# Kernel tuning notes

Hardware: AMD Instinct MI355X
Metric: run time of the kernel (lower is better)

The kernel has to match this reference:

```python
import jax, jax.numpy as jnp
import numpy as np

B, N, NH, E = 4, 4096, 16, 64
MD, FF, H, PE = 128, 256, 4, 32
DH = MD // H
SCALE = 1.0 / np.float32(np.sqrt(DH))


def _ln(x, g, b, eps=1e-5):
    m = jnp.mean(x, axis=-1, keepdims=True)
    v = jnp.var(x, axis=-1, keepdims=True)
    return (x - m) * jax.lax.rsqrt(v + eps) * g + b


def setup_inputs() -> dict:
    key = jax.random.key(0)
    ks = jax.random.split(key, 16)
    rn = lambda k, shape: jax.random.normal(k, shape, dtype=jnp.float32) * 0.02
    return {
        "x": jax.random.normal(ks[0], (B, N, NH, E), dtype=jnp.float32),
        "pos1": jax.random.normal(ks[1], (B, N, NH, NH), dtype=jnp.float32),
        "pos2": jax.random.normal(ks[2], (B, N, NH, NH), dtype=jnp.float32),
        # input_mlp: Linear(E->MD, no bias) + LayerNorm
        "W_in": rn(ks[3], (E, MD)), "g_in": jnp.ones((MD,), jnp.float32), "b_in": jnp.zeros((MD,), jnp.float32),
        # pos_embedder (simple MLP on stacked rel-coords) + emb_proj_bias (PE->H, no bias)
        "W_pe": rn(ks[4], (2, PE)),
        "W_bias": rn(ks[5], (PE, H)),
        # MHA qkv projections (with bias) and output projection
        "Wq": rn(ks[6], (MD, MD)), "bq": jnp.zeros((MD,), jnp.float32),
        "Wk": rn(ks[7], (MD, MD)), "bk": jnp.zeros((MD,), jnp.float32),
        "Wv": rn(ks[8], (MD, MD)), "bv": jnp.zeros((MD,), jnp.float32),
        "Wo": rn(ks[9], (MD, MD)), "bo": jnp.zeros((MD,), jnp.float32),
        # mlp_layer: Linear(MD->FF,no bias), SiLU, Linear(FF->MD,no bias)
        "W1": rn(ks[10], (MD, FF)), "W2": rn(ks[11], (FF, MD)),
        "g1": jnp.ones((MD,), jnp.float32), "b1": jnp.zeros((MD,), jnp.float32),
        "g2": jnp.ones((MD,), jnp.float32), "b2": jnp.zeros((MD,), jnp.float32),
    }


def reference(x, pos1, pos2, W_in, g_in, b_in, W_pe, W_bias,
              Wq, bq, Wk, bk, Wv, bv, Wo, bo, W1, W2, g1, b1, g2, b2):
    b, n, nh, _ = x.shape
    # input_mlp
    h = _ln(x @ W_in, g_in, b_in)                      # [b,n,nh,MD]
    t = h.reshape(b * n, nh, MD)                       # windows of nh tokens
    # relative-position bias: pos_embedder then emb_proj_bias
    pe = jax.nn.silu(jnp.stack([pos1, pos2], axis=-1).reshape(b * n, nh, nh, 2) @ W_pe)  # [bn,nh,nh,PE]
    bias = pe @ W_bias                                  # [bn,nh,nh,H]
    # MHA with additive bias
    q = (t @ Wq + bq).reshape(b * n, nh, H, DH)
    k = (t @ Wk + bk).reshape(b * n, nh, H, DH)
    v = (t @ Wv + bv).reshape(b * n, nh, H, DH)
    scores = jnp.einsum('bqhd,bkhd->bhqk', q, k) * SCALE + jnp.transpose(bias, (0, 3, 1, 2))
    att = jax.nn.softmax(scores, axis=-1)               # [bn,H,nh,nh]
    o = jnp.einsum('bhqk,bkhd->bqhd', att, v).reshape(b * n, nh, MD)
    att_out = o @ Wo + bo
    # residual (q_res=True, dropout=0) + norms + FFN
    y = _ln(t + att_out, g1, b1)
    y = _ln(y + jax.nn.silu(y @ W1) @ W2, g2, b2)
    return y.reshape(b, n, nh, MD)
```

## Files before the change

### kernel.cpp

```cpp
#include <hip/hip_runtime.h>
#include <hip/hip_bf16.h>
#include <math.h>

#define NHT 16
#define MD 128
#define FFD 256
#define NHEAD 4
#define DH 32
#define PED 32
#define ED 64
#define SCALE 0.17677669529663687f
#define SCB 136
#define LDT 132
#define SCUF 264

typedef __attribute__((ext_vector_type(8))) short bf8;
typedef __attribute__((ext_vector_type(4))) float f32x4;
union U8 { bf8 v; unsigned short s[8]; uint u[4]; uint4 q; };

#define MFMA __builtin_amdgcn_mfma_f32_16x16x32_bf16

__device__ __forceinline__ unsigned short bf1(float a){
  __hip_bfloat16 h = __float2bfloat16(a);
  return *reinterpret_cast<unsigned short*>(&h);
}
__device__ __forceinline__ float bfh2f(unsigned short s){
  __hip_bfloat16 h = *reinterpret_cast<__hip_bfloat16*>(&s);
  return __bfloat162float(h);
}
__device__ __forceinline__ float silu_f(float x){ return x / (1.f + __expf(-x)); }

__device__ __forceinline__ void lnC(float (&C)[8][4], const float* __restrict__ g,
                                    const float* __restrict__ b, int lm){
#pragma unroll
  for (int r = 0; r < 4; ++r){
    float s = 0.f, ss = 0.f;
#pragma unroll
    for (int nt = 0; nt < 8; ++nt){ s += C[nt][r]; ss = fmaf(C[nt][r], C[nt][r], ss); }
#pragma unroll
    for (int m = 1; m < 16; m <<= 1){ s += __shfl_xor(s, m); ss += __shfl_xor(ss, m); }
    float mean = s * (1.f/128.f);
    float var  = ss * (1.f/128.f) - mean*mean;
    float rs   = rsqrtf(var + 1e-5f);
#pragma unroll
    for (int nt = 0; nt < 8; ++nt)
      C[nt][r] = fmaf((C[nt][r] - mean) * rs, g[nt*16+lm], b[nt*16+lm]);
  }
}

__global__ __launch_bounds__(256)
void packw(const float* __restrict__ Wq, const float* __restrict__ Wk,
           const float* __restrict__ Wv, const float* __restrict__ Wo,
           const float* __restrict__ W1, const float* __restrict__ W2,
           uint4* __restrict__ ws){
  int id = blockIdx.x * 256 + threadIdx.x;
  const float* W; int KT, N, u; uint4* dst;
  if      (id < 2048) { W = Wq;  KT = 4; N = 128; dst = ws;         u = id;         }
  else if (id < 4096) { W = Wk;  KT = 4; N = 128; dst = ws + 2048;  u = id - 2048;  }
  else if (id < 6144) { W = Wv;  KT = 4; N = 128; dst = ws + 4096;  u = id - 4096;  }
  else if (id < 8192) { W = Wo;  KT = 4; N = 128; dst = ws + 6144;  u = id - 6144;  }
  else if (id < 12288){ W = W1;  KT = 4; N = 256; dst = ws + 8192;  u = id - 8192;  }
  else                { W = W2;  KT = 8; N = 128; dst = ws + 12288; u = id - 12288; }
  int lane = u & 63, tile = u >> 6;
  int kt = tile % KT, nt = tile / KT;
  int kr  = kt*32 + ((lane >> 4) << 3);
  int col = nt*16 + (lane & 15);
  const float* p = W + (size_t)kr * N + col;
  U8 hi;
#pragma unroll
  for (int j = 0; j < 8; ++j) hi.s[j] = bf1(p[(size_t)j * N]);
  dst[u] = hi.q;
}

__global__ __launch_bounds__(256)
void packwin(const float* __restrict__ Win, uint4* __restrict__ ws){
  int u = blockIdx.x * 256 + threadIdx.x;
  int lane = u & 63, tile = u >> 6;
  int kt = tile % 2, nt = tile / 2;
  int kr  = kt*32 + ((lane >> 4) << 3);
  int col = nt*16 + (lane & 15);
  const float* p = Win + (size_t)kr * MD + col;
  U8 hi;
#pragma unroll
  for (int j = 0; j < 8; ++j) hi.s[j] = bf1(p[(size_t)j * MD]);
  ws[16384 + u] = hi.q;
}

__global__ __launch_bounds__(64)
void nha_mfma(const float* __restrict__ x, const float* __restrict__ pos1,
              const float* __restrict__ pos2,
              const float* __restrict__ W_in,
              const float* __restrict__ g_in, const float* __restrict__ b_in,
              const float* __restrict__ W_pe, const float* __restrict__ W_bias,
              const float* __restrict__ bq, const float* __restrict__ bk,
              const float* __restrict__ bv, const float* __restrict__ bo,
              const float* __restrict__ g1, const float* __restrict__ b1,
              const float* __restrict__ g2, const float* __restrict__ b2,
              const uint4* __restrict__ wsp, int useWin, float* __restrict__ out)
{
  const uint4* pWq  = wsp;
  const uint4* pWk  = wsp + 2048;
  const uint4* pWv  = wsp + 4096;
  const uint4* pWo  = wsp + 6144;
  const uint4* pW1  = wsp + 8192;
  const uint4* pW2  = wsp + 12288;
  const uint4* pWin = wsp + 16384;

  __shared__ __align__(16) unsigned short Qb[NHT*SCB];
  __shared__ __align__(16) float Kf[NHT*LDT];
  __shared__ __align__(16) float Vf[NHT*LDT];
  __shared__ __align__(16) unsigned short Tb[NHT*SCB];
  __shared__ __align__(16) unsigned short Ub[NHT*SCUF];
  __shared__ __align__(16) float Bsm[NHEAD*NHT*NHT];

  const int tid = threadIdx.x;
  const int wi  = blockIdx.x;
  const int lm  = tid & 15;
  const int lg  = tid >> 4;
  const f32x4 zero4 = {0.f,0.f,0.f,0.f};

  bf8 xA[2];
  {
    const float* xp = x + (size_t)wi*1024 + lm*ED + lg*8;
#pragma unroll
    for (int kt = 0; kt < 2; ++kt){
      U8 h;
#pragma unroll
      for (int j = 0; j < 8; ++j) h.s[j] = bf1(xp[kt*32 + j]);
      xA[kt] = h.v;
    }
  }
  float tC[8][4];
#pragma unroll
  for (int nt = 0; nt < 8; ++nt){
    f32x4 acc = zero4;
#pragma unroll
    for (int kt = 0; kt < 2; ++kt){
      U8 w;
      if (useWin){
        w.q = pWin[(nt*2+kt)*64 + tid];
      } else {
        const float* wp = W_in + (size_t)(kt*32 + lg*8)*MD + nt*16 + lm;
#pragma unroll
        for (int j = 0; j < 8; ++j) w.s[j] = bf1(wp[(size_t)j*MD]);
      }
      acc = MFMA(xA[kt], w.v, acc, 0,0,0);
    }
#pragma unroll
    for (int r = 0; r < 4; ++r) tC[nt][r] = acc[r];
  }
  lnC(tC, g_in, b_in, lm);

#pragma unroll
  for (int nt = 0; nt < 8; ++nt)
#pragma unroll
    for (int r = 0; r < 4; ++r)
      Tb[(lg*4+r)*SCB + nt*16+lm] = bf1(tC[nt][r]);
  __syncthreads();
  bf8 tA[4];
#pragma unroll
  for (int kt = 0; kt < 4; ++kt)
    tA[kt] = *(const bf8*)(Tb + lm*SCB + kt*32 + lg*8);
  __syncthreads();

#pragma unroll
  for (int nt = 0; nt < 8; ++nt){
    float bb = bq[nt*16+lm];
    f32x4 acc = {bb,bb,bb,bb};
#pragma unroll
    for (int kt = 0; kt < 4; ++kt){
      U8 bh; bh.q = pWq[(nt*4+kt)*64 + tid];
      acc = MFMA(tA[kt], bh.v, acc, 0,0,0);
    }
#pragma unroll
    for (int r = 0; r < 4; ++r) Qb[(lg*4+r)*SCB + nt*16+lm] = bf1(acc[r]);
  }
#pragma unroll
  for (int nt = 0; nt < 8; ++nt){
    float bb = bk[nt*16+lm];
    f32x4 acc = {bb,bb,bb,bb};
#pragma unroll
    for (int kt = 0; kt < 4; ++kt){
      U8 bh; bh.q = pWk[(nt*4+kt)*64 + tid];
      acc = MFMA(tA[kt], bh.v, acc, 0,0,0);
    }
#pragma unroll
    for (int r = 0; r < 4; ++r) Kf[(lg*4+r)*LDT + nt*16+lm] = acc[r];
  }
#pragma unroll
  for (int nt = 0; nt < 8; ++nt){
    float bb = bv[nt*16+lm];
    f32x4 acc = {bb,bb,bb,bb};
#pragma unroll
    for (int kt = 0; kt < 4; ++kt){
      U8 bh; bh.q = pWv[(nt*4+kt)*64 + tid];
      acc = MFMA(tA[kt], bh.v, acc, 0,0,0);
    }
#pragma unroll
    for (int r = 0; r < 4; ++r) Vf[(lg*4+r)*LDT + nt*16+lm] = acc[r];
  }

  for (int p = tid; p < NHT*NHT; p += 64){
    float p1 = pos1[(size_t)wi*256 + p];
    float p2 = pos2[(size_t)wi*256 + p];
    float a0=0.f, a1=0.f, a2=0.f, a3=0.f;
#pragma unroll
    for (int i = 0; i < PED; ++i){
      float e = fmaf(p1, W_pe[i], p2 * W_pe[PED+i]);
      float sv = silu_f(e);
      a0 = fmaf(sv, W_bias[i*4+0], a0);
      a1 = fmaf(sv, W_bias[i*4+1], a1);
      a2 = fmaf(sv, W_bias[i*4+2], a2);
      a3 = fmaf(sv, W_bias[i*4+3], a3);
    }
    Bsm[0*256 + p] = a0; Bsm[1*256 + p] = a1; Bsm[2*256 + p] = a2; Bsm[3*256 + p] = a3;
  }
  __syncthreads();

  {
    const int h  = tid >> 4;
    const int qi = tid & 15;
    float qf[DH];
    {
      const unsigned short* qp = Qb + qi*SCB + h*DH;
#pragma unroll
      for (int d0 = 0; d0 < DH; d0 += 8){
        U8 u; u.v = *(const bf8*)(qp + d0);
#pragma unroll
        for (int j = 0; j < 8; ++j) qf[d0+j] = bfh2f(u.s[j]);
      }
    }
    float sc[NHT];
#pragma unroll
    for (int ki = 0; ki < NHT; ++ki){
      const float* krow = Kf + ki*LDT + h*DH;
      float dot = 0.f;
#pragma unroll
      for (int d = 0; d < DH; d += 4){
        float4 kv = *(const float4*)(krow + d);
        dot = fmaf(qf[d], kv.x, dot);   dot = fmaf(qf[d+1], kv.y, dot);
        dot = fmaf(qf[d+2], kv.z, dot); dot = fmaf(qf[d+3], kv.w, dot);
      }
      sc[ki] = fmaf(dot, SCALE, Bsm[h*256 + qi*16 + ki]);
    }
    float mx = sc[0];
#pragma unroll
    for (int ki = 1; ki < NHT; ++ki) mx = fmaxf(mx, sc[ki]);
    float sum = 0.f;
#pragma unroll
    for (int ki = 0; ki < NHT; ++ki){ sc[ki] = __expf(sc[ki]-mx); sum += sc[ki]; }
    const float inv = 1.f/sum;
    float of[DH];
#pragma unroll
    for (int d = 0; d < DH; ++d) of[d] = 0.f;
#pragma unroll
    for (int ki = 0; ki < NHT; ++ki){
      const float* vrow = Vf + ki*LDT + h*DH;
      const float a = sc[ki];
#pragma unroll
      for (int d = 0; d < DH; d += 4){
        float4 vv = *(const float4*)(vrow + d);
        of[d]   = fmaf(a, vv.x, of[d]);   of[d+1] = fmaf(a, vv.y, of[d+1]);
        of[d+2] = fmaf(a, vv.z, of[d+2]); of[d+3] = fmaf(a, vv.w, of[d+3]);
      }
    }
    unsigned short* op_ = Qb + qi*SCB + h*DH;
#pragma unroll
    for (int d = 0; d < DH; ++d) op_[d] = bf1(of[d]*inv);
  }
  __syncthreads();

  bf8 oA[4];
#pragma unroll
  for (int kt = 0; kt < 4; ++kt)
    oA[kt] = *(const bf8*)(Qb + lm*SCB + kt*32 + lg*8);
#pragma unroll
  for (int nt = 0; nt < 8; ++nt){
    float bb = bo[nt*16+lm];
    f32x4 acc = {bb,bb,bb,bb};
#pragma unroll
    for (int kt = 0; kt < 4; ++kt){
      U8 bh; bh.q = pWo[(nt*4+kt)*64 + tid];
      acc = MFMA(oA[kt], bh.v, acc, 0,0,0);
    }
#pragma unroll
    for (int r = 0; r < 4; ++r) tC[nt][r] += acc[r];
  }
  lnC(tC, g1, b1, lm);
  __syncthreads();

#pragma unroll
  for (int nt = 0; nt < 8; ++nt)
#pragma unroll
    for (int r = 0; r < 4; ++r)
      Tb[(lg*4+r)*SCB + nt*16+lm] = bf1(tC[nt][r]);
  __syncthreads();
  bf8 yA[4];
#pragma unroll
  for (int kt = 0; kt < 4; ++kt)
    yA[kt] = *(const bf8*)(Tb + lm*SCB + kt*32 + lg*8);
  __syncthreads();

#pragma unroll
  for (int nt1 = 0; nt1 < 16; ++nt1){
    f32x4 a = zero4;
#pragma unroll
    for (int kt = 0; kt < 4; ++kt){
      U8 bh; bh.q = pW1[(nt1*4+kt)*64 + tid];
      a = MFMA(yA[kt], bh.v, a, 0,0,0);
    }
#pragma unroll
    for (int r = 0; r < 4; ++r)
      Ub[(lg*4+r)*SCUF + nt1*16 + lm] = bf1(silu_f(a[r]));
  }
  __syncthreads();
  f32x4 acc2[8];
#pragma unroll
  for (int nt = 0; nt < 8; ++nt) acc2[nt] = zero4;
#pragma unroll
  for (int kt2 = 0; kt2 < 8; ++kt2){
    bf8 uA = *(const bf8*)(Ub + lm*SCUF + kt2*32 + lg*8);
#pragma unroll
    for (int nt = 0; nt < 8; ++nt){
      U8 bh; bh.q = pW2[(nt*8+kt2)*64 + tid];
      acc2[nt] = MFMA(uA, bh.v, acc2[nt], 0,0,0);
    }
  }

#pragma unroll
  for (int nt = 0; nt < 8; ++nt)
#pragma unroll
    for (int r = 0; r < 4; ++r) tC[nt][r] += acc2[nt][r];
  lnC(tC, g2, b2, lm);

  float* op = out + (size_t)wi*(NHT*MD);
#pragma unroll
  for (int nt = 0; nt < 8; ++nt)
#pragma unroll
    for (int r = 0; r < 4; ++r)
      op[(lg*4+r)*MD + nt*16+lm] = tC[nt][r];
}

extern "C" void kernel_launch(void* const* d_in, const int* in_sizes, int n_in,
                              void* d_out, int out_size, void* d_ws, size_t ws_size,
                              hipStream_t stream) {
  const float* x     = (const float*)d_in[0];
  const float* pos1  = (const float*)d_in[1];
  const float* pos2  = (const float*)d_in[2];
  const float* W_in  = (const float*)d_in[3];
  const float* g_in  = (const float*)d_in[4];
  const float* b_in  = (const float*)d_in[5];
  const float* W_pe  = (const float*)d_in[6];
  const float* W_bias= (const float*)d_in[7];
  const float* Wq    = (const float*)d_in[8];
  const float* bq    = (const float*)d_in[9];
  const float* Wk    = (const float*)d_in[10];
  const float* bk    = (const float*)d_in[11];
  const float* Wv    = (const float*)d_in[12];
  const float* bv    = (const float*)d_in[13];
  const float* Wo    = (const float*)d_in[14];
  const float* bo    = (const float*)d_in[15];
  const float* W1    = (const float*)d_in[16];
  const float* W2    = (const float*)d_in[17];
  const float* g1    = (const float*)d_in[18];
  const float* b1    = (const float*)d_in[19];
  const float* g2    = (const float*)d_in[20];
  const float* b2    = (const float*)d_in[21];
  float* out = (float*)d_out;
  uint4* ws  = (uint4*)d_ws;

  const int useWin = (ws_size >= (size_t)(16384 + 1024) * 16) ? 1 : 0;

  packw<<<64, 256, 0, stream>>>(Wq, Wk, Wv, Wo, W1, W2, ws);
  if (useWin) packwin<<<4, 256, 0, stream>>>(W_in, ws);

  const int nwin = in_sizes[0] / (NHT * ED);
  nha_mfma<<<nwin, 64, 0, stream>>>(x, pos1, pos2, W_in, g_in, b_in, W_pe, W_bias,
                                    bq, bk, bv, bo, g1, b1, g2, b2, ws, useWin, out);
}
```

Baseline: 448.5 us.

## Compute windowed attention scores and PV with bf16 MFMA instead of scalar FMA

Replaces the per-thread scalar QK dot products and PV accumulation with 16x16x32 bf16 MFMA instructions. K is stored as bf16 and V is stored transposed as bf16, and the softmax runs on the MFMA output layout using cross-lane shuffles. Probabilities are staged in a new LDS buffer, and the K dimension is zero-padded in the PV MFMA. SiLU now uses a fast reciprocal. This cuts VALU work and LDS traffic in the attention phase, at the cost of extra shuffles, a barrier, and lower K/V/P precision.

```diff
diff --git a/kernel.cpp b/kernel.cpp
--- a/kernel.cpp
+++ b/kernel.cpp
@@ -11,7 +11,6 @@
 #define ED 64
 #define SCALE 0.17677669529663687f
 #define SCB 136
-#define LDT 132
 #define SCUF 264
 
 typedef __attribute__((ext_vector_type(8))) short bf8;
@@ -28,7 +27,9 @@
   __hip_bfloat16 h = *reinterpret_cast<__hip_bfloat16*>(&s);
   return __bfloat162float(h);
 }
-__device__ __forceinline__ float silu_f(float x){ return x / (1.f + __expf(-x)); }
+__device__ __forceinline__ float silu_f(float x){
+  return x * __builtin_amdgcn_rcpf(1.f + __expf(-x));
+}
 
 __device__ __forceinline__ void lnC(float (&C)[8][4], const float* __restrict__ g,
                                     const float* __restrict__ b, int lm){
@@ -107,8 +108,9 @@
   const uint4* pWin = wsp + 16384;
 
   __shared__ __align__(16) unsigned short Qb[NHT*SCB];
-  __shared__ __align__(16) float Kf[NHT*LDT];
-  __shared__ __align__(16) float Vf[NHT*LDT];
+  __shared__ __align__(16) unsigned short Kb[NHT*SCB];
+  __shared__ __align__(16) unsigned short Vt[MD*NHT];
+  __shared__ __align__(16) unsigned short Pb[NHT*SCB];
   __shared__ __align__(16) unsigned short Tb[NHT*SCB];
   __shared__ __align__(16) unsigned short Ub[NHT*SCUF];
   __shared__ __align__(16) float Bsm[NHEAD*NHT*NHT];
@@ -118,6 +120,7 @@
   const int lm  = tid & 15;
   const int lg  = tid >> 4;
   const f32x4 zero4 = {0.f,0.f,0.f,0.f};
+  const bf8  zero8 = {0,0,0,0,0,0,0,0};
 
   bf8 xA[2];
   {
@@ -185,7 +188,7 @@
       acc = MFMA(tA[kt], bh.v, acc, 0,0,0);
     }
 #pragma unroll
-    for (int r = 0; r < 4; ++r) Kf[(lg*4+r)*LDT + nt*16+lm] = acc[r];
+    for (int r = 0; r < 4; ++r) Kb[(lg*4+r)*SCB + nt*16+lm] = bf1(acc[r]);
   }
 #pragma unroll
   for (int nt = 0; nt < 8; ++nt){
@@ -197,7 +200,7 @@
       acc = MFMA(tA[kt], bh.v, acc, 0,0,0);
     }
 #pragma unroll
-    for (int r = 0; r < 4; ++r) Vf[(lg*4+r)*LDT + nt*16+lm] = acc[r];
+    for (int r = 0; r < 4; ++r) Vt[(nt*16+lm)*NHT + lg*4+r] = bf1(acc[r]);
   }
 
   for (int p = tid; p < NHT*NHT; p += 64){
@@ -217,56 +220,43 @@
   }
   __syncthreads();
 
-  {
-    const int h  = tid >> 4;
-    const int qi = tid & 15;
-    float qf[DH];
-    {
-      const unsigned short* qp = Qb + qi*SCB + h*DH;
-#pragma unroll
-      for (int d0 = 0; d0 < DH; d0 += 8){
-        U8 u; u.v = *(const bf8*)(qp + d0);
-#pragma unroll
-        for (int j = 0; j < 8; ++j) qf[d0+j] = bfh2f(u.s[j]);
-      }
-    }
-    float sc[NHT];
-#pragma unroll
-    for (int ki = 0; ki < NHT; ++ki){
-      const float* krow = Kf + ki*LDT + h*DH;
-      float dot = 0.f;
-#pragma unroll
-      for (int d = 0; d < DH; d += 4){
-        float4 kv = *(const float4*)(krow + d);
-        dot = fmaf(qf[d], kv.x, dot);   dot = fmaf(qf[d+1], kv.y, dot);
-        dot = fmaf(qf[d+2], kv.z, dot); dot = fmaf(qf[d+3], kv.w, dot);
-      }
-      sc[ki] = fmaf(dot, SCALE, Bsm[h*256 + qi*16 + ki]);
-    }
-    float mx = sc[0];
-#pragma unroll
-    for (int ki = 1; ki < NHT; ++ki) mx = fmaxf(mx, sc[ki]);
-    float sum = 0.f;
-#pragma unroll
-    for (int ki = 0; ki < NHT; ++ki){ sc[ki] = __expf(sc[ki]-mx); sum += sc[ki]; }
-    const float inv = 1.f/sum;
-    float of[DH];
-#pragma unroll
-    for (int d = 0; d < DH; ++d) of[d] = 0.f;
-#pragma unroll
-    for (int ki = 0; ki < NHT; ++ki){
-      const float* vrow = Vf + ki*LDT + h*DH;
-      const float a = sc[ki];
-#pragma unroll
-      for (int d = 0; d < DH; d += 4){
-        float4 vv = *(const float4*)(vrow + d);
-        of[d]   = fmaf(a, vv.x, of[d]);   of[d+1] = fmaf(a, vv.y, of[d+1]);
-        of[d+2] = fmaf(a, vv.z, of[d+2]); of[d+3] = fmaf(a, vv.w, of[d+3]);
-      }
-    }
-    unsigned short* op_ = Qb + qi*SCB + h*DH;
-#pragma unroll
-    for (int d = 0; d < DH; ++d) op_[d] = bf1(of[d]*inv);
+  bf8 qA[4], kB[4];
+#pragma unroll
+  for (int h = 0; h < 4; ++h){
+    qA[h] = *(const bf8*)(Qb + lm*SCB + h*32 + lg*8);
+    kB[h] = *(const bf8*)(Kb + lm*SCB + h*32 + lg*8);
+  }
+#pragma unroll
+  for (int h = 0; h < 4; ++h){
+    f32x4 s = MFMA(qA[h], kB[h], zero4, 0,0,0);
+#pragma unroll
+    for (int r = 0; r < 4; ++r){
+      float v = fmaf(s[r], SCALE, Bsm[h*256 + (lg*4+r)*16 + lm]);
+      float mx = v;
+#pragma unroll
+      for (int m = 1; m < 16; m <<= 1) mx = fmaxf(mx, __shfl_xor(mx, m));
+      float e = __expf(v - mx);
+      float sm = e;
+#pragma unroll
+      for (int m = 1; m < 16; m <<= 1) sm += __shfl_xor(sm, m);
+      Pb[(lg*4+r)*SCB + h*32 + lm] = bf1(e * __builtin_amdgcn_rcpf(sm));
+    }
+  }
+  __syncthreads();
+
+#pragma unroll
+  for (int h = 0; h < 4; ++h){
+    bf8 aP = *(const bf8*)(Pb + lm*SCB + h*32 + lg*8);
+    if (tid >= 32) aP = zero8;
+#pragma unroll
+    for (int n2 = 0; n2 < 2; ++n2){
+      bf8 vB = *(const bf8*)(Vt + (h*32 + n2*16 + lm)*NHT + (lg & 1)*8);
+      if (tid >= 32) vB = zero8;
+      f32x4 o = MFMA(aP, vB, zero4, 0,0,0);
+#pragma unroll
+      for (int r = 0; r < 4; ++r)
+        Qb[(lg*4+r)*SCB + h*32 + n2*16 + lm] = bf1(o[r]);
+    }
   }
   __syncthreads();
 
```

Result: faster. 386.7 us, median of 3 (-13.8%).
